# Performance work log

Hardware: AMD Instinct MI355X
Metric: run time of the kernel (lower is better)

## Reference

```python
import jax, jax.numpy as jnp
import numpy as np
from jax import lax


def setup_inputs() -> dict:
    key = jax.random.key(0)
    ks = jax.random.split(key, 8)
    B, L, H = 2, 1024, 2048
    E = 2
    d = H * E            # d_inner = 4096
    S = 16               # state_dim
    R = 128              # dt_rank = ceil(H / 16)
    sc = lambda fan_in: 1.0 / np.sqrt(fan_in)
    return {
        "x": jax.random.normal(ks[0], (B, L, H), jnp.float32),
        "W_in": jax.random.normal(ks[1], (H, 2 * d), jnp.float32) * sc(H),
        "conv_w": jax.random.normal(ks[2], (d, 1, 3), jnp.float32) * sc(3),
        "conv_b": jnp.zeros((d,), jnp.float32),
        "W_x": jax.random.normal(ks[3], (d, R + 2 * S), jnp.float32) * sc(d),
        "W_dt": jax.random.normal(ks[4], (R, d), jnp.float32) * sc(R),
        "b_dt": jnp.zeros((d,), jnp.float32),
        "A_log": jnp.log(jnp.tile(jnp.arange(1, S + 1, dtype=jnp.float32), (d, 1))),
        "D": jnp.ones((d,), jnp.float32),
        "W_out": jax.random.normal(ks[5], (d, H), jnp.float32) * sc(d),
    }


def reference(x, W_in, conv_w, conv_b, W_x, W_dt, b_dt, A_log, D, W_out):
    d = conv_b.shape[0]
    S = A_log.shape[1]
    R = W_dt.shape[0]
    # in_proj and gate split
    xz = x @ W_in                              # [B, L, 2d]
    xp, z = jnp.split(xz, 2, axis=-1)          # each [B, L, d]
    # depthwise conv1d (kernel 3, pad 1)
    xc = lax.conv_general_dilated(
        jnp.transpose(xp, (0, 2, 1)), conv_w, (1,), [(1, 1)],
        feature_group_count=d, dimension_numbers=("NCH", "OIH", "NCH"))
    xc = jnp.transpose(xc + conv_b[None, :, None], (0, 2, 1))  # [B, L, d]
    xc = jax.nn.silu(xc)
    # x_proj -> dt, B, C
    x_dbl = xc @ W_x                           # [B, L, R + 2S]
    dt_in = x_dbl[..., :R]
    Bm = x_dbl[..., R:R + S]                   # [B, L, S]
    Cm = x_dbl[..., R + S:]                    # [B, L, S]
    dt = jax.nn.softplus(dt_in @ W_dt + b_dt)  # [B, L, d]
    A = -jnp.exp(A_log)                        # [d, S]

    def step(h, ins):
        u_t, dt_t, B_t, C_t = ins              # [B,d], [B,d], [B,S], [B,S]
        dA = jnp.exp(dt_t[:, :, None] * A)     # [B, d, S]
        h = dA * h + dt_t[:, :, None] * B_t[:, None, :] * u_t[:, :, None]
        y_t = jnp.einsum("bds,bs->bd", h, C_t)
        return h, y_t

    h0 = jnp.zeros((x.shape[0], d, S), xc.dtype)
    xsT = (jnp.swapaxes(xc, 0, 1), jnp.swapaxes(dt, 0, 1),
           jnp.swapaxes(Bm, 0, 1), jnp.swapaxes(Cm, 0, 1))
    _, yT = lax.scan(step, h0, xsT)            # yT: [L, B, d]
    y = jnp.swapaxes(yT, 0, 1) + xc * D        # skip connection
    y = y * jax.nn.silu(z)                     # gate
    return y @ W_out                           # [B, L, H]
```

## Files before the change

### kernel.cpp

```cpp
#include <hip/hip_runtime.h>
#include <hip/hip_bf16.h>


using u16 = unsigned short;
typedef __bf16 bf16x8 __attribute__((ext_vector_type(8)));
typedef float f32x4 __attribute__((ext_vector_type(4)));
typedef u16 u16x8 __attribute__((ext_vector_type(8)));

#define NCHUNK 16
#define CLEN   64
#define SWZ(row, q) ((q) ^ (((row) >> 1) & 3))

__device__ __forceinline__ float bf2f(u16 u) {
    union { unsigned int i; float f; } v; v.i = ((unsigned int)u) << 16; return v.f;
}
__device__ __forceinline__ u16 f2bf(float f) {
    union { float f; unsigned int i; } v; v.f = f;
    unsigned int x = v.i;
    return (u16)((x + 0x7FFFu + ((x >> 16) & 1u)) >> 16);
}

__device__ __forceinline__ float* hloc_ptr(u16* xzbase, int i) {
    return reinterpret_cast<float*>(xzbase + (size_t)(i >> 11) * 8192) + (i & 2047);
}
__device__ __forceinline__ float* hin_ptr(u16* xzbase, int i) {
    return reinterpret_cast<float*>(xzbase + (size_t)((i >> 11) + 1024) * 8192) + (i & 2047);
}

__global__ void detect_dtype(const u16* __restrict__ xraw, int* __restrict__ flag) {
    __shared__ int cnt[256];
    const int tid = threadIdx.x;
    int plausible = 0;
    for (int i = tid; i < 4096; i += 256) {
        const u16 v = xraw[2 * i];
        const int e = (v >> 7) & 0xFF;
        plausible += (e >= 100 && e <= 145) ? 1 : 0;
    }
    cnt[tid] = plausible;
    __syncthreads();
    for (int s = 128; s > 0; s >>= 1) {
        if (tid < s) cnt[tid] += cnt[tid + s];
        __syncthreads();
    }
    if (tid == 0) *flag = (cnt[0] > 2458) ? 1 : 0;
}

__device__ __forceinline__ void cvt_seg(const void* src, u16* dst, int i,
                                        bool isbf) {
    dst[i] = isbf ? ((const u16*)src)[i] : f2bf(((const float*)src)[i]);
}
__global__ void cvt_fused(const void* __restrict__ x_raw, u16* __restrict__ xcan,
                          const void* __restrict__ cw_raw, u16* __restrict__ cw_c,
                          const void* __restrict__ cb_raw, u16* __restrict__ cb_c,
                          const void* __restrict__ bdt_raw, u16* __restrict__ bdt_c,
                          const void* __restrict__ Alog_raw, u16* __restrict__ Alog_c,
                          const void* __restrict__ D_raw, u16* __restrict__ D_c,
                          float* __restrict__ x_dbl,
                          const int* __restrict__ flag) {
    const bool isbf = (*flag != 0);
    int blk = blockIdx.x;
    const int tid = threadIdx.x;
    if (blk < 16384) { cvt_seg(x_raw, xcan, blk * 256 + tid, isbf); return; }
    blk -= 16384;
    if (blk < 48)  { cvt_seg(cw_raw, cw_c, blk * 256 + tid, isbf); return; }
    blk -= 48;
    if (blk < 16)  { cvt_seg(cb_raw, cb_c, blk * 256 + tid, isbf); return; }
    blk -= 16;
    if (blk < 16)  { cvt_seg(bdt_raw, bdt_c, blk * 256 + tid, isbf); return; }
    blk -= 16;
    if (blk < 256) { cvt_seg(Alog_raw, Alog_c, blk * 256 + tid, isbf); return; }
    blk -= 256;
    if (blk < 16)  { cvt_seg(D_raw, D_c, blk * 256 + tid, isbf); return; }
    blk -= 16;
    x_dbl[blk * 256 + tid] = 0.f;
}

__device__ __forceinline__ void tr_tile(const void* in, u16* out, int R, int C,
                                        int bx, int by, int tx, int ty, bool isbf,
                                        u16 (*tile)[33]) {
    const int c0 = bx * 32, r0 = by * 64;
#pragma unroll
    for (int i = 0; i < 8; i++) {
        const int rl = ty + i * 8;
        const size_t idx = (size_t)(r0 + rl) * C + c0 + tx;
        tile[rl][tx] = isbf ? ((const u16*)in)[idx]
                            : f2bf(((const float*)in)[idx]);
    }
    __syncthreads();
#pragma unroll
    for (int i = 0; i < 4; i++) {
        const int w = ty + i * 8;
        union { u16 h[2]; unsigned int u; } p;
        p.h[0] = tile[2 * tx][w];
        p.h[1] = tile[2 * tx + 1][w];
        *reinterpret_cast<unsigned int*>(&out[(size_t)(c0 + w) * R + r0 + 2 * tx]) = p.u;
    }
}
__global__ void transpose_fused(const void* __restrict__ Wi, u16* __restrict__ WiT,
                                const void* __restrict__ Wo, u16* __restrict__ WoT,
                                const void* __restrict__ Wd, u16* __restrict__ WdT,
                                const void* __restrict__ Wx, u16* __restrict__ WxT,
                                const int* __restrict__ flag) {
    __shared__ u16 tile[64][33];
    const bool isbf = (*flag != 0);
    const int tx = threadIdx.x, ty = threadIdx.y;
    int blk = blockIdx.x;
    if (blk < 8192) { tr_tile(Wi, WiT, 2048, 8192, blk % 256, blk / 256, tx, ty, isbf, tile); return; }
    blk -= 8192;
    if (blk < 4096) { tr_tile(Wo, WoT, 4096, 2048, blk % 64, blk / 64, tx, ty, isbf, tile); return; }
    blk -= 4096;
    if (blk < 256)  { tr_tile(Wd, WdT, 128, 4096, blk % 128, blk / 128, tx, ty, isbf, tile); return; }
    blk -= 256;
    tr_tile(Wx, WxT, 4096, 160, blk % 5, blk / 5, tx, ty, isbf, tile);
}

template <int BM, int BN, int THR>
__device__ __forceinline__ void stage_ring(const u16* __restrict__ Ab,
                                           const u16* __restrict__ Bb,
                                           int K, int k0, u16* dst, int tid)
{
    constexpr int CHA = BM * 4, CHB = BN * 4;
    static_assert(CHA % THR == 0 && CHB % THR == 0, "chunk/thread mismatch");
#pragma unroll
    for (int it = 0; it < CHA / THR; it++) {
        const int c = it * THR + tid;
        const int row = c >> 2, kc = SWZ(row, c & 3);
        __builtin_amdgcn_global_load_lds(
            (const __attribute__((address_space(1))) void*)(Ab + (size_t)row * K + k0 + kc * 8),
            (__attribute__((address_space(3))) void*)(dst + c * 8), 16, 0, 0);
    }
#pragma unroll
    for (int it = 0; it < CHB / THR; it++) {
        const int c = it * THR + tid;
        const int row = c >> 2, kc = SWZ(row, c & 3);
        __builtin_amdgcn_global_load_lds(
            (const __attribute__((address_space(1))) void*)(Bb + (size_t)row * K + k0 + kc * 8),
            (__attribute__((address_space(3))) void*)(dst + BM * 32 + c * 8), 16, 0, 0);
    }
}

template <int BM, int BN, int WM, int WN, int MODE>
__global__ __launch_bounds__(64 * WM * WN, 2) void gemm_ring(
    const u16* __restrict__ A, const u16* __restrict__ Bt, void* __restrict__ C,
    const int* __restrict__ oflagp, int M, int N, int K)
{
    constexpr int THR = 64 * WM * WN;
    constexpr int MT  = BM / (WM * 16);
    constexpr int NT  = BN / (WN * 16);
    constexpr int NPH = 2;
    constexpr int GM  = MT / NPH;
    constexpr int STG = (BM + BN) * 32;
    static_assert((BM * 4 + BN * 4) / THR == 4, "vmcnt ladder assumes 4 loads/thread/stage");
    static_assert(MT % NPH == 0, "MT must split into NPH phases");
    extern __shared__ u16 smem[];

    const int tid  = threadIdx.x;
    const int lane = tid & 63;
    const int wave = tid >> 6;
    const int wm = wave / WN, wn = wave % WN;
    const int q  = lane >> 4;
    const int n0 = blockIdx.x * BN;
    const int m0 = blockIdx.y * BM;
    const int NTILE = K >> 5;

    const u16* Ab = A  + (size_t)m0 * K;
    const u16* Bb = Bt + (size_t)n0 * K;

    stage_ring<BM, BN, THR>(Ab, Bb, K, 0,  smem + 0 * STG, tid);
    stage_ring<BM, BN, THR>(Ab, Bb, K, 32, smem + 1 * STG, tid);
    stage_ring<BM, BN, THR>(Ab, Bb, K, 64, smem + 2 * STG, tid);

    f32x4 acc[MT][NT];
#pragma unroll
    for (int mi = 0; mi < MT; mi++)
#pragma unroll
        for (int ni = 0; ni < NT; ni++)
            acc[mi][ni] = (f32x4){0.f, 0.f, 0.f, 0.f};

    const int arow = wm * (MT * 16) + (lane & 15);
    const int brow = wn * (NT * 16) + (lane & 15);

    for (int t = 0; t < NTILE; t++) {
        const int tp = t + 3;
        if (tp < NTILE) {
            stage_ring<BM, BN, THR>(Ab, Bb, K, tp * 32, smem + (tp & 3) * STG, tid);
            asm volatile("s_waitcnt vmcnt(12)" ::: "memory");
        } else if (tp == NTILE) {
            asm volatile("s_waitcnt vmcnt(8)" ::: "memory");
        } else if (tp == NTILE + 1) {
            asm volatile("s_waitcnt vmcnt(4)" ::: "memory");
        } else {
            asm volatile("s_waitcnt vmcnt(0)" ::: "memory");
        }
        __builtin_amdgcn_s_barrier();

        const u16* As = smem + (t & 3) * STG;
        const u16* Bs = As + BM * 32;
        bf16x8 bfr[NT];
#pragma unroll
        for (int ni = 0; ni < NT; ni++) {
            const int r = brow + ni * 16;
            bfr[ni] = *reinterpret_cast<const bf16x8*>(&Bs[r * 32 + SWZ(r, q) * 8]);
        }
#pragma unroll
        for (int g = 0; g < NPH; g++) {
            bf16x8 af[GM];
#pragma unroll
            for (int i = 0; i < GM; i++) {
                const int r = arow + (g * GM + i) * 16;
                af[i] = *reinterpret_cast<const bf16x8*>(&As[r * 32 + SWZ(r, q) * 8]);
            }
            __builtin_amdgcn_s_setprio(1);
#pragma unroll
            for (int i = 0; i < GM; i++)
#pragma unroll
                for (int ni = 0; ni < NT; ni++)
                    acc[g * GM + i][ni] = __builtin_amdgcn_mfma_f32_16x16x32_bf16(
                        af[i], bfr[ni], acc[g * GM + i][ni], 0, 0, 0);
            __builtin_amdgcn_s_setprio(0);
            __builtin_amdgcn_sched_barrier(0);
            __builtin_amdgcn_s_barrier();
        }
    }

    int oflag = 1;
    if constexpr (MODE == 1) oflag = *oflagp;

    const int rb = m0 + wm * (MT * 16) + (q << 2);
    const int cb = n0 + wn * (NT * 16) + (lane & 15);
#pragma unroll
    for (int mi = 0; mi < MT; mi++) {
#pragma unroll
        for (int ni = 0; ni < NT; ni++) {
            const int col = cb + ni * 16;
#pragma unroll
            for (int r = 0; r < 4; r++) {
                const int row = rb + mi * 16 + r;
                const float v = acc[mi][ni][r];
                if constexpr (MODE == 0) {
                    ((u16*)C)[(size_t)row * N + col] = f2bf(v);
                } else {
                    if (oflag) ((u16*)C)[(size_t)row * N + col] = f2bf(v);
                    else       ((float*)C)[(size_t)row * N + col] = v;
                }
            }
        }
    }
}

template <int BM, int BN, int BK, int WR, int WC, int MT, int NT, int MODE>
__global__ __launch_bounds__(256) void gemm_bt(
    const u16* __restrict__ A, const u16* __restrict__ Bt,
    void* __restrict__ C, const u16* __restrict__ bias,
    const int* __restrict__ oflagp,
    int M, int N, int K)
{
    static_assert(BK == 32, "BK=32 (one 16x16x32 MFMA k-slab)");
    __shared__ u16 As[BM * BK];
    __shared__ u16 Bs[BN * BK];

    const int tid  = threadIdx.x;
    const int lane = tid & 63;
    const int wave = tid >> 6;
    const int wm = wave / WC, wn = wave % WC;

    const int m0 = blockIdx.y * BM;
    const int n0 = blockIdx.x * BN;
    const int Kchunk = K / gridDim.z;
    const int kbeg = blockIdx.z * Kchunk;
    const int kend = kbeg + Kchunk;

    f32x4 acc[MT][NT];
#pragma unroll
    for (int mi = 0; mi < MT; mi++)
#pragma unroll
        for (int ni = 0; ni < NT; ni++)
            acc[mi][ni] = (f32x4){0.f, 0.f, 0.f, 0.f};

    const int q = lane >> 4;
    const int arow = wm * MT * 16 + (lane & 15);
    const int brow = wn * NT * 16 + (lane & 15);

    constexpr int CHA = BM * 4;
    constexpr int CHB = BN * 4;

    for (int k0 = kbeg; k0 < kend; k0 += BK) {
        __syncthreads();
#pragma unroll
        for (int it = 0; it < (CHA + 255) / 256; it++) {
            const int c = it * 256 + tid;
            if (CHA % 256 == 0 || c < CHA) {
                const int row = c >> 2, kc = SWZ(row, c & 3);
                const u16* gp = &A[(size_t)(m0 + row) * K + k0 + kc * 8];
                __builtin_amdgcn_global_load_lds(
                    (const __attribute__((address_space(1))) void*)gp,
                    (__attribute__((address_space(3))) void*)&As[c * 8], 16, 0, 0);
            }
        }
#pragma unroll
        for (int it = 0; it < (CHB + 255) / 256; it++) {
            const int c = it * 256 + tid;
            if (CHB % 256 == 0 || c < CHB) {
                const int row = c >> 2, kc = SWZ(row, c & 3);
                const u16* gp = &Bt[(size_t)(n0 + row) * K + k0 + kc * 8];
                __builtin_amdgcn_global_load_lds(
                    (const __attribute__((address_space(1))) void*)gp,
                    (__attribute__((address_space(3))) void*)&Bs[c * 8], 16, 0, 0);
            }
        }
        __syncthreads();

        bf16x8 af[MT], bfr[NT];
#pragma unroll
        for (int mi = 0; mi < MT; mi++) {
            const int row = arow + mi * 16;
            af[mi] = *reinterpret_cast<const bf16x8*>(&As[row * BK + SWZ(row, q) * 8]);
        }
#pragma unroll
        for (int ni = 0; ni < NT; ni++) {
            const int row = brow + ni * 16;
            bfr[ni] = *reinterpret_cast<const bf16x8*>(&Bs[row * BK + SWZ(row, q) * 8]);
        }
#pragma unroll
        for (int mi = 0; mi < MT; mi++)
#pragma unroll
            for (int ni = 0; ni < NT; ni++)
                acc[mi][ni] = __builtin_amdgcn_mfma_f32_16x16x32_bf16(
                    af[mi], bfr[ni], acc[mi][ni], 0, 0, 0);
    }

    const int rb = m0 + wm * MT * 16 + ((lane >> 4) << 2);
    const int cb = n0 + wn * NT * 16 + (lane & 15);
#pragma unroll
    for (int mi = 0; mi < MT; mi++) {
#pragma unroll
        for (int ni = 0; ni < NT; ni++) {
            const int col = cb + ni * 16;
#pragma unroll
            for (int r = 0; r < 4; r++) {
                const int row = rb + mi * 16 + r;
                const float v = acc[mi][ni][r];
                if constexpr (MODE == 0) {
                    ((u16*)C)[(size_t)row * N + col] = f2bf(v);
                } else if constexpr (MODE == 4) {
                    atomicAdd(((float*)C) + (size_t)row * N + col, v);
                }
            }
        }
    }
}

__global__ __launch_bounds__(256) void dt_gemm(
    const u16* __restrict__ A,
    const u16* __restrict__ Bt,
    float* __restrict__ C,
    const u16* __restrict__ bias)
{
    __shared__ ulong4 smem_raw[2048];
    u16* As = (u16*)smem_raw;
    u16* Bs = As + 64 * 128;
    float* Cs = (float*)smem_raw;

    const int tid  = threadIdx.x;
    const int lane = tid & 63;
    const int wave = tid >> 6;
    const int n0 = blockIdx.x * 64;
    const int m0 = blockIdx.y * 64;

#pragma unroll
    for (int it = 0; it < 4; it++) {
        const int c = it * 256 + tid;
        const int row = c >> 4, cc = (c & 15) ^ (row & 7);
        const u16* gp = &A[(size_t)(m0 + row) * 128 + cc * 8];
        __builtin_amdgcn_global_load_lds(
            (const __attribute__((address_space(1))) void*)gp,
            (__attribute__((address_space(3))) void*)&As[c * 8], 16, 0, 0);
    }
#pragma unroll
    for (int it = 0; it < 4; it++) {
        const int c = it * 256 + tid;
        const int row = c >> 4, cc = (c & 15) ^ (row & 7);
        const u16* gp = &Bt[(size_t)(n0 + row) * 128 + cc * 8];
        __builtin_amdgcn_global_load_lds(
            (const __attribute__((address_space(1))) void*)gp,
            (__attribute__((address_space(3))) void*)&Bs[c * 8], 16, 0, 0);
    }
    __syncthreads();

    const int q  = lane >> 4;
    const int ar = wave * 16 + (lane & 15);
    f32x4 acc[4];
#pragma unroll
    for (int ni = 0; ni < 4; ni++) acc[ni] = (f32x4){0.f, 0.f, 0.f, 0.f};

#pragma unroll
    for (int kk = 0; kk < 4; kk++) {
        const int cA = kk * 4 + q;
        const bf16x8 af = *reinterpret_cast<const bf16x8*>(
            &As[(ar * 16 + (cA ^ (ar & 7))) * 8]);
#pragma unroll
        for (int ni = 0; ni < 4; ni++) {
            const int br = ni * 16 + (lane & 15);
            const bf16x8 bfr = *reinterpret_cast<const bf16x8*>(
                &Bs[(br * 16 + (cA ^ (br & 7))) * 8]);
            acc[ni] = __builtin_amdgcn_mfma_f32_16x16x32_bf16(af, bfr, acc[ni], 0, 0, 0);
        }
    }
    __syncthreads();

#pragma unroll
    for (int ni = 0; ni < 4; ni++) {
        const int col = ni * 16 + (lane & 15);
#pragma unroll
        for (int r = 0; r < 4; r++) {
            const int rowl = wave * 16 + q * 4 + r;
            Cs[rowl * 68 + col] = acc[ni][r];
        }
    }
    __syncthreads();

#pragma unroll
    for (int p = 0; p < 4; p++) {
        const int rowl = p * 16 + (tid >> 4);
        const int c0 = (tid & 15) * 4;
        float4 v = *reinterpret_cast<const float4*>(&Cs[rowl * 68 + c0]);
        float* vp = reinterpret_cast<float*>(&v);
#pragma unroll
        for (int j = 0; j < 4; j++) {
            const float x = vp[j] + bf2f(bias[n0 + c0 + j]);
            vp[j] = fmaxf(x, 0.f) + __logf(1.f + __expf(-fabsf(x)));
        }
        *reinterpret_cast<float4*>(&C[(size_t)(m0 + rowl) * 4096 + n0 + c0]) = v;
    }
}

__global__ void conv_silu(const u16* __restrict__ xz, const u16* __restrict__ conv_w,
                          const u16* __restrict__ conv_b, u16* __restrict__ xc) {
    const int idx = blockIdx.x * 256 + threadIdx.x;
    const int row = idx >> 9, c0 = (idx & 511) * 8;
    const int l = row & 1023;

    u16 wcat[24];
    *(u16x8*)&wcat[0]  = *(const u16x8*)&conv_w[c0 * 3];
    *(u16x8*)&wcat[8]  = *(const u16x8*)&conv_w[c0 * 3 + 8];
    *(u16x8*)&wcat[16] = *(const u16x8*)&conv_w[c0 * 3 + 16];
    const u16x8 bv = *(const u16x8*)&conv_b[c0];
    const u16x8 x0 = *(const u16x8*)&xz[(size_t)row * 8192 + c0];
    u16x8 xm = {}, xp = {};
    if (l > 0)    xm = *(const u16x8*)&xz[(size_t)(row - 1) * 8192 + c0];
    if (l < 1023) xp = *(const u16x8*)&xz[(size_t)(row + 1) * 8192 + c0];

    u16x8 out;
#pragma unroll
    for (int i = 0; i < 8; i++) {
        float v = bf2f(wcat[3 * i]) * bf2f(xm[i])
                + bf2f(wcat[3 * i + 1]) * bf2f(x0[i])
                + bf2f(wcat[3 * i + 2]) * bf2f(xp[i])
                + bf2f(bv[i]);
        v = v / (1.f + __expf(-v));
        out[i] = f2bf(v);
    }
    *(u16x8*)&xc[(size_t)row * 4096 + c0] = out;
}

__global__ void cvt_dtin(const float* __restrict__ x_dbl, u16* __restrict__ dtin) {
    const int idx = blockIdx.x * 256 + threadIdx.x;
    const int row = idx >> 7, c = idx & 127;
    dtin[idx] = f2bf(x_dbl[(size_t)row * 160 + c]);
}

__global__ __launch_bounds__(256) void scan_p1(
    const float* __restrict__ dt, const u16* __restrict__ xc,
    const float* __restrict__ x_dbl, const u16* __restrict__ A_log,
    float* __restrict__ Parr, u16* __restrict__ xzbase)
{
    __shared__ float Bsm[CLEN][16];
    const int tid = threadIdx.x;
    const int nc = blockIdx.x, cg = blockIdx.y, b = blockIdx.z;
    const int ch = cg * 256 + tid;
    const size_t row0 = (size_t)b * 1024 + nc * CLEN;

    {
        const int t = tid >> 2, q = tid & 3;
        const float4 v = *(const float4*)&x_dbl[(row0 + t) * 160 + 128 + q * 4];
        *(float4*)&Bsm[t][q * 4] = v;
    }
    __syncthreads();

    float A_s[16], h[16];
#pragma unroll
    for (int s = 0; s < 16; s++) {
        A_s[s] = -__expf(bf2f(A_log[ch * 16 + s]));
        h[s] = 0.f;
    }
    float Sdt = 0.f;

    float dt_v = dt[row0 * 4096 + ch];
    float u_v  = bf2f(xc[row0 * 4096 + ch]);
    for (int t = 0; t < CLEN; t++) {
        const int tn = (t + 1 < CLEN) ? t + 1 : t;
        const float dt_n = dt[(row0 + tn) * 4096 + ch];
        const float u_n  = bf2f(xc[(row0 + tn) * 4096 + ch]);
        const float dtu = dt_v * u_v;
        Sdt += dt_v;
        const f32x4* Brow = (const f32x4*)&Bsm[t][0];
        const f32x4 B0 = Brow[0], B1 = Brow[1], B2 = Brow[2], B3 = Brow[3];
#pragma unroll
        for (int s = 0; s < 16; s++) {
            const float Bs_ = (s < 4 ? B0[s & 3] : s < 8 ? B1[s & 3] : s < 12 ? B2[s & 3] : B3[s & 3]);
            const float dA = __expf(dt_v * A_s[s]);
            h[s] = dA * h[s] + dtu * Bs_;
        }
        dt_v = dt_n; u_v = u_n;
    }
    const int i0 = (((b * NCHUNK + nc) * 4096) + ch) * 16;
    float* pp = &Parr[i0];
    float* hp = hloc_ptr(xzbase, i0);
#pragma unroll
    for (int s4 = 0; s4 < 4; s4++) {
        float4 pq, hq;
        pq.x = __expf(A_s[4 * s4 + 0] * Sdt);
        pq.y = __expf(A_s[4 * s4 + 1] * Sdt);
        pq.z = __expf(A_s[4 * s4 + 2] * Sdt);
        pq.w = __expf(A_s[4 * s4 + 3] * Sdt);
        hq.x = h[4 * s4 + 0]; hq.y = h[4 * s4 + 1];
        hq.z = h[4 * s4 + 2]; hq.w = h[4 * s4 + 3];
        *(float4*)&pp[4 * s4] = pq;
        *(float4*)&hp[4 * s4] = hq;
    }
}

__global__ __launch_bounds__(256) void scan_p2(
    const float* __restrict__ Parr, u16* __restrict__ xzbase)
{
    const int tid = threadIdx.x;
    const int lane = tid & 63, wave = tid >> 6;
    const int blk = blockIdx.x;
    const int b = blk >> 8, cg = blk & 255;
    const int c_local = lane & 3, s = lane >> 2;
    const int ch = cg * 16 + wave * 4 + c_local;

    float Pv[NCHUNK], hl[NCHUNK];
#pragma unroll
    for (int c = 0; c < NCHUNK; c++) {
        const int i = (((b * NCHUNK + c) * 4096) + ch) * 16 + s;
        Pv[c] = Parr[i];
        hl[c] = *hloc_ptr(xzbase, i);
    }
    float hin = 0.f;
#pragma unroll
    for (int c = 0; c < NCHUNK; c++) {
        const int i = (((b * NCHUNK + c) * 4096) + ch) * 16 + s;
        *hin_ptr(xzbase, i) = hin;
        hin = Pv[c] * hin + hl[c];
    }
}

__global__ __launch_bounds__(256) void scan_p3(
    const float* __restrict__ dt, const u16* __restrict__ xc,
    const float* __restrict__ x_dbl, const u16* __restrict__ xz,
    const u16* __restrict__ A_log, const u16* __restrict__ Dp,
    u16* __restrict__ yg, u16* __restrict__ xzbase)
{
    __shared__ float BCs[CLEN][32];
    const int tid = threadIdx.x;
    const int nc = blockIdx.x, cg = blockIdx.y, b = blockIdx.z;
    const int ch = cg * 256 + tid;
    const size_t row0 = (size_t)b * 1024 + nc * CLEN;

#pragma unroll
    for (int it = 0; it < 2; it++) {
        const int c = it * 256 + tid;
        const int t = c >> 3, q = c & 7;
        const float4 v = *(const float4*)&x_dbl[(row0 + t) * 160 + 128 + q * 4];
        *(float4*)&BCs[t][q * 4] = v;
    }
    __syncthreads();

    float A_s[16], h[16];
    const int i0 = (((b * NCHUNK + nc) * 4096) + ch) * 16;
    {
        const float* hp = hin_ptr(xzbase, i0);
#pragma unroll
        for (int s4 = 0; s4 < 4; s4++) {
            const float4 hq = *(const float4*)&hp[4 * s4];
            h[4 * s4 + 0] = hq.x; h[4 * s4 + 1] = hq.y;
            h[4 * s4 + 2] = hq.z; h[4 * s4 + 3] = hq.w;
        }
    }
#pragma unroll
    for (int s = 0; s < 16; s++)
        A_s[s] = -__expf(bf2f(A_log[ch * 16 + s]));
    const float D_ch = bf2f(Dp[ch]);

    float dt_v = dt[row0 * 4096 + ch];
    float u_v  = bf2f(xc[row0 * 4096 + ch]);
    float z_v  = bf2f(xz[row0 * 8192 + 4096 + ch]);
    for (int t = 0; t < CLEN; t++) {
        const int tn = (t + 1 < CLEN) ? t + 1 : t;
        const size_t rn = row0 + tn;
        const float dt_n = dt[rn * 4096 + ch];
        const float u_n  = bf2f(xc[rn * 4096 + ch]);
        const float z_n  = bf2f(xz[rn * 8192 + 4096 + ch]);
        const float dtu = dt_v * u_v;

        const f32x4* Row = (const f32x4*)&BCs[t][0];
        const f32x4 B0 = Row[0], B1 = Row[1], B2 = Row[2], B3 = Row[3];
        const f32x4 C0 = Row[4], C1 = Row[5], C2 = Row[6], C3 = Row[7];

        float y0 = 0.f, y1 = 0.f, y2 = 0.f, y3 = 0.f;
#pragma unroll
        for (int s = 0; s < 16; s++) {
            const float Bs_ = (s < 4 ? B0[s & 3] : s < 8 ? B1[s & 3] : s < 12 ? B2[s & 3] : B3[s & 3]);
            const float Cs_ = (s < 4 ? C0[s & 3] : s < 8 ? C1[s & 3] : s < 12 ? C2[s & 3] : C3[s & 3]);
            const float dA = __expf(dt_v * A_s[s]);
            h[s] = dA * h[s] + dtu * Bs_;
            const float hc = h[s] * Cs_;
            if ((s & 3) == 0) y0 += hc; else if ((s & 3) == 1) y1 += hc;
            else if ((s & 3) == 2) y2 += hc; else y3 += hc;
        }
        const float y = (y0 + y1) + (y2 + y3);
        const float silu_z = z_v / (1.f + __expf(-z_v));
        yg[(row0 + t) * 4096 + ch] = f2bf((y + u_v * D_ch) * silu_z);
        dt_v = dt_n; u_v = u_n; z_v = z_n;
    }
}

extern "C" void kernel_launch(void* const* d_in, const int* in_sizes, int n_in,
                              void* d_out, int out_size, void* d_ws, size_t ws_size,
                              hipStream_t stream)
{
    const void* x_raw      = d_in[0];
    const void* W_in_raw   = d_in[1];
    const void* conv_w_raw = d_in[2];
    const void* conv_b_raw = d_in[3];
    const void* W_x_raw    = d_in[4];
    const void* W_dt_raw   = d_in[5];
    const void* b_dt_raw   = d_in[6];
    const void* A_log_raw  = d_in[7];
    const void* D_raw      = d_in[8];
    const void* W_out_raw  = d_in[9];

    char* ws = (char*)d_ws;
    size_t off = 0;
    auto alloc = [&](size_t bytes) { char* p = ws + off; off += (bytes + 255) & ~(size_t)255; return p; };
    int*   flag   = (int*)  alloc(4);
    u16*   W_inT  = (u16*)  alloc(8192ULL * 2048 * 2);
    u16*   W_outT = (u16*)  alloc(2048ULL * 4096 * 2);
    u16*   W_dtT  = (u16*)  alloc(4096ULL * 128 * 2);
    u16*   W_xT   = (u16*)  alloc(160ULL * 4096 * 2);
    u16*   xz     = (u16*)  alloc(2048ULL * 8192 * 2);
    u16*   xc     = (u16*)  alloc(2048ULL * 4096 * 2);
    float* x_dbl  = (float*)alloc(2048ULL * 160 * 4);
    u16*   dtin   = (u16*)  alloc(2048ULL * 128 * 2);
    u16*   yg     = (u16*)  alloc(2048ULL * 4096 * 2);
    u16*   xcan   = (u16*)  alloc(2048ULL * 2048 * 2);
    u16*   cw_c   = (u16*)  alloc(12288 * 2);
    u16*   cb_c   = (u16*)  alloc(4096 * 2);
    u16*   bdt_c  = (u16*)  alloc(4096 * 2);
    u16*   Alog_c = (u16*)  alloc(65536 * 2);
    u16*   D_c    = (u16*)  alloc(4096 * 2);
    float* dtv    = (float*)W_inT;
    float* Parr   = (float*)xcan;

    detect_dtype<<<1, 256, 0, stream>>>((const u16*)x_raw, flag);
    cvt_fused<<<16384 + 48 + 16 + 16 + 256 + 16 + 1280, 256, 0, stream>>>(
        x_raw, xcan, conv_w_raw, cw_c, conv_b_raw, cb_c, b_dt_raw, bdt_c,
        A_log_raw, Alog_c, D_raw, D_c, x_dbl, flag);

    transpose_fused<<<8192 + 4096 + 256 + 320, dim3(32, 8), 0, stream>>>(
        W_in_raw, W_inT, W_out_raw, W_outT, W_dt_raw, W_dtT, W_x_raw, W_xT, flag);

    (void)hipFuncSetAttribute(
        reinterpret_cast<const void*>(&gemm_ring<256, 256, 2, 4, 0>),
        hipFuncAttributeMaxDynamicSharedMemorySize, 131072);
    gemm_ring<256, 256, 2, 4, 0><<<dim3(8192 / 256, 2048 / 256), 512, 131072, stream>>>(
        xcan, W_inT, xz, nullptr, 2048, 8192, 2048);

    conv_silu<<<(2048 * 512) / 256, 256, 0, stream>>>(xz, cw_c, cb_c, xc);

    gemm_bt<64, 160, 32, 4, 1, 1, 10, 4>
        <<<dim3(1, 2048 / 64, 8), 256, 0, stream>>>(xc, W_xT, x_dbl, nullptr, nullptr, 2048, 160, 4096);

    cvt_dtin<<<(2048 * 128) / 256, 256, 0, stream>>>(x_dbl, dtin);

    dt_gemm<<<dim3(4096 / 64, 2048 / 64), 256, 0, stream>>>(dtin, W_dtT, dtv, bdt_c);

    scan_p1<<<dim3(NCHUNK, 16, 2), 256, 0, stream>>>(dtv, xc, x_dbl, Alog_c, Parr, xz);
    scan_p2<<<512, 256, 0, stream>>>(Parr, xz);
    scan_p3<<<dim3(NCHUNK, 16, 2), 256, 0, stream>>>(dtv, xc, x_dbl, xz, Alog_c, D_c, yg, xz);

    (void)hipFuncSetAttribute(
        reinterpret_cast<const void*>(&gemm_ring<128, 128, 2, 2, 1>),
        hipFuncAttributeMaxDynamicSharedMemorySize, 65536);
    gemm_ring<128, 128, 2, 2, 1><<<dim3(2048 / 128, 2048 / 128), 256, 65536, stream>>>(
        yg, W_outT, d_out, flag, 2048, 2048, 4096);
}
```

Baseline: 430.2 us.

## Replace split-K atomics with partial buffers and vectorize conversion kernels

The x_proj split-K GEMM now writes each K-slice's partial result to its own buffer instead of doing float atomicAdd into a zeroed x_dbl. A new reduce kernel sums the eight partials and also emits the bf16 dt input, which removes both the zero-fill and the separate cvt_dtin kernel. The input conversion kernels are vectorized to eight elements per thread, and the transpose loads now read two elements per thread. In exchange the code needs an extra 10 MB partial buffer and pays for reading it back in the reduce step.

```diff
diff --git a/kernel.cpp b/kernel.cpp
--- a/kernel.cpp
+++ b/kernel.cpp
@@ -45,9 +45,17 @@
     if (tid == 0) *flag = (cnt[0] > 2458) ? 1 : 0;
 }
 
-__device__ __forceinline__ void cvt_seg(const void* src, u16* dst, int i,
-                                        bool isbf) {
-    dst[i] = isbf ? ((const u16*)src)[i] : f2bf(((const float*)src)[i]);
+__device__ __forceinline__ void cvt_seg8(const void* src, u16* dst, int i8,
+                                         bool isbf) {
+    if (isbf) {
+        *(u16x8*)&dst[i8 * 8] = *((const u16x8*)src + i8);
+    } else {
+        const float* f = (const float*)src + i8 * 8;
+        u16x8 o;
+#pragma unroll
+        for (int j = 0; j < 8; j++) o[j] = f2bf(f[j]);
+        *(u16x8*)&dst[i8 * 8] = o;
+    }
 }
 __global__ void cvt_fused(const void* __restrict__ x_raw, u16* __restrict__ xcan,
                           const void* __restrict__ cw_raw, u16* __restrict__ cw_c,
@@ -55,36 +63,42 @@
                           const void* __restrict__ bdt_raw, u16* __restrict__ bdt_c,
                           const void* __restrict__ Alog_raw, u16* __restrict__ Alog_c,
                           const void* __restrict__ D_raw, u16* __restrict__ D_c,
-                          float* __restrict__ x_dbl,
                           const int* __restrict__ flag) {
     const bool isbf = (*flag != 0);
     int blk = blockIdx.x;
     const int tid = threadIdx.x;
-    if (blk < 16384) { cvt_seg(x_raw, xcan, blk * 256 + tid, isbf); return; }
-    blk -= 16384;
-    if (blk < 48)  { cvt_seg(cw_raw, cw_c, blk * 256 + tid, isbf); return; }
-    blk -= 48;
-    if (blk < 16)  { cvt_seg(cb_raw, cb_c, blk * 256 + tid, isbf); return; }
-    blk -= 16;
-    if (blk < 16)  { cvt_seg(bdt_raw, bdt_c, blk * 256 + tid, isbf); return; }
-    blk -= 16;
-    if (blk < 256) { cvt_seg(Alog_raw, Alog_c, blk * 256 + tid, isbf); return; }
-    blk -= 256;
-    if (blk < 16)  { cvt_seg(D_raw, D_c, blk * 256 + tid, isbf); return; }
-    blk -= 16;
-    x_dbl[blk * 256 + tid] = 0.f;
+    if (blk < 2048) { cvt_seg8(x_raw, xcan, blk * 256 + tid, isbf); return; }
+    blk -= 2048;
+    if (blk < 6)  { cvt_seg8(cw_raw, cw_c, blk * 256 + tid, isbf); return; }
+    blk -= 6;
+    if (blk < 2)  { cvt_seg8(cb_raw, cb_c, blk * 256 + tid, isbf); return; }
+    blk -= 2;
+    if (blk < 2)  { cvt_seg8(bdt_raw, bdt_c, blk * 256 + tid, isbf); return; }
+    blk -= 2;
+    if (blk < 32) { cvt_seg8(Alog_raw, Alog_c, blk * 256 + tid, isbf); return; }
+    blk -= 32;
+    cvt_seg8(D_raw, D_c, blk * 256 + tid, isbf);
 }
 
 __device__ __forceinline__ void tr_tile(const void* in, u16* out, int R, int C,
                                         int bx, int by, int tx, int ty, bool isbf,
-                                        u16 (*tile)[33]) {
+                                        u16 (*tile)[34]) {
     const int c0 = bx * 32, r0 = by * 64;
-#pragma unroll
-    for (int i = 0; i < 8; i++) {
-        const int rl = ty + i * 8;
-        const size_t idx = (size_t)(r0 + rl) * C + c0 + tx;
-        tile[rl][tx] = isbf ? ((const u16*)in)[idx]
-                            : f2bf(((const float*)in)[idx]);
+    const int cp = tx & 15, rh = tx >> 4;
+#pragma unroll
+    for (int i = 0; i < 4; i++) {
+        const int row = ty + rh * 8 + i * 16;
+        const size_t idx = (size_t)(r0 + row) * C + c0 + cp * 2;
+        if (isbf) {
+            union { unsigned int u; u16 h[2]; } p;
+            p.u = *reinterpret_cast<const unsigned int*>(&((const u16*)in)[idx]);
+            tile[row][cp * 2] = p.h[0];
+            tile[row][cp * 2 + 1] = p.h[1];
+        } else {
+            const float2 f = *reinterpret_cast<const float2*>(&((const float*)in)[idx]);
+            tile[row][cp * 2] = f2bf(f.x);
+            tile[row][cp * 2 + 1] = f2bf(f.y);
+        }
     }
     __syncthreads();
 #pragma unroll
@@ -101,7 +115,7 @@
                                 const void* __restrict__ Wd, u16* __restrict__ WdT,
                                 const void* __restrict__ Wx, u16* __restrict__ WxT,
                                 const int* __restrict__ flag) {
-    __shared__ u16 tile[64][33];
+    __shared__ u16 tile[64][34];
     const bool isbf = (*flag != 0);
     const int tx = threadIdx.x, ty = threadIdx.y;
     int blk = blockIdx.x;
@@ -342,12 +356,23 @@
                 const float v = acc[mi][ni][r];
                 if constexpr (MODE == 0) {
                     ((u16*)C)[(size_t)row * N + col] = f2bf(v);
-                } else if constexpr (MODE == 4) {
-                    atomicAdd(((float*)C) + (size_t)row * N + col, v);
+                } else if constexpr (MODE == 5) {
+                    ((float*)C)[((size_t)blockIdx.z * M + row) * N + col] = v;
                 }
             }
         }
     }
+}
+
+__global__ void reduce_xdbl(const float* __restrict__ part,
+                            float* __restrict__ x_dbl, u16* __restrict__ dtin) {
+    const int idx = blockIdx.x * 256 + threadIdx.x;
+    const int row = idx / 160, col = idx - row * 160;
+    float s = 0.f;
+#pragma unroll
+    for (int z = 0; z < 8; z++) s += part[(size_t)z * (2048 * 160) + idx];
+    x_dbl[idx] = s;
+    if (col < 128) dtin[row * 128 + col] = f2bf(s);
 }
 
 __global__ __launch_bounds__(256) void dt_gemm(
@@ -461,12 +486,6 @@
         out[i] = f2bf(v);
     }
     *(u16x8*)&xc[(size_t)row * 4096 + c0] = out;
-}
-
-__global__ void cvt_dtin(const float* __restrict__ x_dbl, u16* __restrict__ dtin) {
-    const int idx = blockIdx.x * 256 + threadIdx.x;
-    const int row = idx >> 7, c = idx & 127;
-    dtin[idx] = f2bf(x_dbl[(size_t)row * 160 + c]);
 }
 
 __global__ __launch_bounds__(256) void scan_p1(
@@ -655,6 +674,7 @@
     u16*   dtin   = (u16*)  alloc(2048ULL * 128 * 2);
     u16*   yg     = (u16*)  alloc(2048ULL * 4096 * 2);
     u16*   xcan   = (u16*)  alloc(2048ULL * 2048 * 2);
+    float* xdblp  = (float*)alloc(8ULL * 2048 * 160 * 4);
     u16*   cw_c   = (u16*)  alloc(12288 * 2);
     u16*   cb_c   = (u16*)  alloc(4096 * 2);
     u16*   bdt_c  = (u16*)  alloc(4096 * 2);
@@ -664,9 +684,9 @@
     float* Parr   = (float*)xcan;
 
     detect_dtype<<<1, 256, 0, stream>>>((const u16*)x_raw, flag);
-    cvt_fused<<<16384 + 48 + 16 + 16 + 256 + 16 + 1280, 256, 0, stream>>>(
+    cvt_fused<<<2048 + 6 + 2 + 2 + 32 + 2, 256, 0, stream>>>(
         x_raw, xcan, conv_w_raw, cw_c, conv_b_raw, cb_c, b_dt_raw, bdt_c,
-        A_log_raw, Alog_c, D_raw, D_c, x_dbl, flag);
+        A_log_raw, Alog_c, D_raw, D_c, flag);
 
     transpose_fused<<<8192 + 4096 + 256 + 320, dim3(32, 8), 0, stream>>>(
         W_in_raw, W_inT, W_out_raw, W_outT, W_dt_raw, W_dtT, W_x_raw, W_xT, flag);
@@ -679,10 +699,10 @@
 
     conv_silu<<<(2048 * 512) / 256, 256, 0, stream>>>(xz, cw_c, cb_c, xc);
 
-    gemm_bt<64, 160, 32, 4, 1, 1, 10, 4>
-        <<<dim3(1, 2048 / 64, 8), 256, 0, stream>>>(xc, W_xT, x_dbl, nullptr, nullptr, 2048, 160, 4096);
-
-    cvt_dtin<<<(2048 * 128) / 256, 256, 0, stream>>>(x_dbl, dtin);
+    gemm_bt<64, 160, 32, 4, 1, 1, 10, 5>
+        <<<dim3(1, 2048 / 64, 8), 256, 0, stream>>>(xc, W_xT, xdblp, nullptr, nullptr, 2048, 160, 4096);
+
+    reduce_xdbl<<<(2048 * 160) / 256, 256, 0, stream>>>(xdblp, x_dbl, dtin);
 
     dt_gemm<<<dim3(4096 / 64, 2048 / 64), 256, 0, stream>>>(dtin, W_dtT, dtv, bdt_c);
 
```

Result: faster. 408.8 us (-5.0%).
